# Kernel tuning notes

Hardware: AMD Instinct MI355X
Metric: run time of the kernel (lower is better)

Reference implementation:

```python
import jax, jax.numpy as jnp
import numpy as np

B, D, H, W = 16, 128, 64, 64
K = 512  # num_embeddings


def setup_inputs() -> dict:
    key = jax.random.key(0)
    k1, k2 = jax.random.split(key)
    inputs = jax.random.normal(k1, (B, D, H, W), dtype=jnp.float32)
    embedding_weight = jax.random.normal(k2, (K, D), dtype=jnp.float32)
    return {"inputs": inputs, "embedding_weight": embedding_weight}


def reference(inputs, embedding_weight):
    # NCHW -> NHWC, flatten to [N, D]
    x = jnp.transpose(inputs, (0, 2, 3, 1))  # [B, H, W, D]
    flat = x.reshape(-1, x.shape[-1])        # [N, D]
    dists = (
        jnp.sum(flat ** 2, axis=1, keepdims=True)
        + jnp.sum(embedding_weight ** 2, axis=1)
        - 2.0 * flat @ embedding_weight.T
    )  # [N, K]
    idx = jnp.argmin(dists, axis=1)          # [N]
    # one-hot @ codebook == gather
    quantized = embedding_weight[idx].reshape(x.shape)  # [B, H, W, D]
    # straight-through estimator
    quantized = x + jax.lax.stop_gradient(quantized - x)
    return jnp.transpose(quantized, (0, 3, 1, 2))  # back to NCHW
```

## Files before the change

kernel.cpp:

```cpp
#include <hip/hip_runtime.h>


typedef _Float16 f16;
typedef _Float16 f16x4 __attribute__((ext_vector_type(4)));
typedef _Float16 f16x8 __attribute__((ext_vector_type(8)));
typedef float f32x16 __attribute__((ext_vector_type(16)));

#define ND 128
#define NK 512
#define NHW 4096
#define LO_SCALE 2048.0f
#define LO_INV (1.0f / 2048.0f)

#define WS_EHI 0
#define WS_ELO 131072u
#define WS_ENS 262144u
#define WS_NEED 264192u

__global__ __launch_bounds__(256) void vq_prep_e(const float* __restrict__ e,
                                                 f16* __restrict__ ehi, f16* __restrict__ elo,
                                                 float* __restrict__ ens) {
  const int tid = threadIdx.x;
  const int k0 = (int)blockIdx.x * 16;
  const int r = tid >> 4, dq16 = tid & 15;
  const int k = k0 + r;
  float ssum = 0.0f;
  #pragma unroll
  for (int hh = 0; hh < 2; ++hh) {
    const int dq = dq16 + 16 * hh;
    const float4 v = *(const float4*)(e + (size_t)k * ND + 4 * dq);
    ssum += v.x * v.x + v.y * v.y + v.z * v.z + v.w * v.w;
    float va[4] = {v.x, v.y, v.z, v.w};
    f16x4 hv, lv;
    #pragma unroll
    for (int j = 0; j < 4; ++j) {
      const f16 h = (f16)va[j];
      hv[j] = h;
      lv[j] = (f16)((va[j] - (float)h) * LO_SCALE);
    }
    const int sl = (dq >> 1) ^ (k & 15);
    const size_t off = (size_t)k * ND + sl * 8 + (dq & 1) * 4;
    *(f16x4*)(ehi + off) = hv;
    *(f16x4*)(elo + off) = lv;
  }
  #pragma unroll
  for (int m = 1; m < 16; m <<= 1) ssum += __shfl_xor(ssum, m, 64);
  if (dq16 == 0) ens[k] = 0.5f * ssum;
}

__global__ __launch_bounds__(256) void vq_score(const float* __restrict__ x,
                                                const f16* __restrict__ ehi,
                                                const f16* __restrict__ elo,
                                                const float* __restrict__ ens,
                                                const float* __restrict__ e32,
                                                float* __restrict__ out) {
  __shared__ f16 eh_s[64 * 128];
  __shared__ f16 el_s[64 * 128];
  __shared__ float ens_s[NK];

  const int tid = threadIdx.x;
  const int w = tid >> 6;
  const int lane = tid & 63;
  const int l31 = lane & 31;
  const int half = lane >> 5;
  const int T0 = (int)blockIdx.x * 128;
  const int tok = T0 + w * 32 + l31;
  const int bb = tok >> 12;
  const int hw = tok & 4095;

  #pragma unroll
  for (int p = 0; p < 4; ++p) {
    __builtin_amdgcn_global_load_lds(ehi + p * 2048 + tid * 8, &eh_s[p * 2048 + tid * 8], 16, 0, 0);
    __builtin_amdgcn_global_load_lds(elo + p * 2048 + tid * 8, &el_s[p * 2048 + tid * 8], 16, 0, 0);
  }

  f16x8 Bh[8], Bl[8];
  {
    const float* xb = x + (size_t)bb * ND * NHW + hw;
    #pragma unroll
    for (int ks = 0; ks < 8; ++ks) {
      const int oct = 2 * ks + half;
      #pragma unroll
      for (int j = 0; j < 8; ++j) {
        const float v = xb[(size_t)(oct * 8 + j) * NHW];
        const f16 hv = (f16)v;
        Bh[ks][j] = hv;
        Bl[ks][j] = (f16)((v - (float)hv) * LO_SCALE);
      }
    }
  }
  ens_s[tid] = ens[tid];
  ens_s[tid + 256] = ens[tid + 256];
  __syncthreads();

  float bv = -3.0e38f;
  int bi = 0;
  const int sbase = l31 & 15;

  for (int c = 0; c < 8; ++c) {
    #pragma unroll
    for (int cg = 0; cg < 2; ++cg) {
      const int r = cg * 32 + l31;
      const f16* ah = &eh_s[r * 128];
      const f16* al = &el_s[r * 128];
      f32x16 a1 = {}, a2 = {};
      __builtin_amdgcn_s_setprio(1);
      #pragma unroll
      for (int ks = 0; ks < 8; ++ks) {
        const int sl = ((2 * ks + half) ^ sbase) * 8;
        const f16x8 Ah = *(const f16x8*)(ah + sl);
        const f16x8 Al = *(const f16x8*)(al + sl);
        a2 = __builtin_amdgcn_mfma_f32_32x32x16_f16(Al, Bh[ks], a2, 0, 0, 0);
        a1 = __builtin_amdgcn_mfma_f32_32x32x16_f16(Ah, Bh[ks], a1, 0, 0, 0);
        a2 = __builtin_amdgcn_mfma_f32_32x32x16_f16(Ah, Bl[ks], a2, 0, 0, 0);
      }
      __builtin_amdgcn_s_setprio(0);
      const int kb = c * 64 + cg * 32 + 4 * half;
      const float4 b0 = *(const float4*)&ens_s[kb + 0];
      const float4 b1 = *(const float4*)&ens_s[kb + 8];
      const float4 b2 = *(const float4*)&ens_s[kb + 16];
      const float4 b3 = *(const float4*)&ens_s[kb + 24];
      const float bias[16] = {b0.x, b0.y, b0.z, b0.w, b1.x, b1.y, b1.z, b1.w,
                              b2.x, b2.y, b2.z, b2.w, b3.x, b3.y, b3.z, b3.w};
      #pragma unroll
      for (int rr = 0; rr < 16; ++rr) {
        const float s = a1[rr] + a2[rr] * LO_INV - bias[rr];
        const int code = kb + (rr & 3) + 8 * (rr >> 2);
        if (s > bv) { bv = s; bi = code; }
      }
    }
    __syncthreads();
    if (c < 7) {
      const f16* gh = ehi + (c + 1) * 8192;
      const f16* gl = elo + (c + 1) * 8192;
      #pragma unroll
      for (int p = 0; p < 4; ++p) {
        __builtin_amdgcn_global_load_lds(gh + p * 2048 + tid * 8, &eh_s[p * 2048 + tid * 8], 16, 0, 0);
        __builtin_amdgcn_global_load_lds(gl + p * 2048 + tid * 8, &el_s[p * 2048 + tid * 8], 16, 0, 0);
      }
      __syncthreads();
    }
  }

  {
    const float ov = __shfl_xor(bv, 32, 64);
    const int oi = __shfl_xor(bi, 32, 64);
    if (ov > bv || (ov == bv && oi < bi)) { bv = ov; bi = oi; }
  }

  {
    const float* er = e32 + (size_t)bi * ND + half * 64;
    float* ob = out + (size_t)bb * ND * NHW + (size_t)(half * 64) * NHW + hw;
    #pragma unroll
    for (int j4 = 0; j4 < 16; ++j4) {
      const float4 ev = *(const float4*)(er + j4 * 4);
      ob[(size_t)(j4 * 4 + 0) * NHW] = ev.x;
      ob[(size_t)(j4 * 4 + 1) * NHW] = ev.y;
      ob[(size_t)(j4 * 4 + 2) * NHW] = ev.z;
      ob[(size_t)(j4 * 4 + 3) * NHW] = ev.w;
    }
  }
}

__global__ __launch_bounds__(128) void vq_enorm(const float* __restrict__ e,
                                                float* __restrict__ ensw) {
  const int k = blockIdx.x;
  const int d = threadIdx.x;
  const float v = e[k * ND + d];
  float s = v * v;
  #pragma unroll
  for (int off = 32; off > 0; off >>= 1) s += __shfl_down(s, off, 64);
  __shared__ float tmp[2];
  if ((d & 63) == 0) tmp[d >> 6] = s;
  __syncthreads();
  if (d == 0) ensw[k] = tmp[0] + tmp[1];
}

__global__ __launch_bounds__(256, 2) void vq_main_f32(const float* __restrict__ x,
                                                      const float* __restrict__ e,
                                                      const float* __restrict__ ensw,
                                                      float* __restrict__ out) {
  __shared__ float xs[ND][64];
  __shared__ float esh[ND][64];
  __shared__ float enh[NK];
  __shared__ float red_v[64][17];
  __shared__ int red_i[64][17];
  __shared__ int bidx[64];
  const int tid = threadIdx.x;
  const int b = blockIdx.x >> 6;
  const int hw0 = (blockIdx.x & 63) * 64;
  const float* xb = x + ((size_t)b * ND) * NHW;
  #pragma unroll
  for (int i = 0; i < 8; ++i) {
    const int f = tid + 256 * i;
    const int d = f >> 4, t4 = f & 15;
    const float4 v = *(const float4*)(xb + (size_t)d * NHW + hw0 + 4 * t4);
    *(float4*)&xs[d][4 * t4] = v;
  }
  #pragma unroll
  for (int i = 0; i < 2; ++i) enh[tid + 256 * i] = ensw[tid + 256 * i];
  const int t4 = tid & 15, m = tid >> 4;
  float bvv[4] = {-3.0e38f, -3.0e38f, -3.0e38f, -3.0e38f};
  int bii[4] = {0, 0, 0, 0};
  for (int kc = 0; kc < NK / 64; ++kc) {
    __syncthreads();
    #pragma unroll
    for (int i = 0; i < 8; ++i) {
      const int f = tid + 256 * i;
      const int kk = f & 63, dq = f >> 6;
      const float4 v = *(const float4*)(e + (size_t)(kc * 64 + kk) * ND + 4 * dq);
      esh[4 * dq + 0][kk] = v.x; esh[4 * dq + 1][kk] = v.y;
      esh[4 * dq + 2][kk] = v.z; esh[4 * dq + 3][kk] = v.w;
    }
    __syncthreads();
    float acc[4][4];
    #pragma unroll
    for (int a = 0; a < 4; ++a)
      #pragma unroll
      for (int cc = 0; cc < 4; ++cc) acc[a][cc] = 0.0f;
    #pragma unroll 8
    for (int d = 0; d < ND; ++d) {
      const float4 xv = *(const float4*)&xs[d][4 * t4];
      const float4 ev = *(const float4*)&esh[d][4 * m];
      const float xa[4] = {xv.x, xv.y, xv.z, xv.w};
      const float ea[4] = {ev.x, ev.y, ev.z, ev.w};
      #pragma unroll
      for (int a = 0; a < 4; ++a)
        #pragma unroll
        for (int cc = 0; cc < 4; ++cc) acc[a][cc] = fmaf(xa[a], ea[cc], acc[a][cc]);
    }
    const int kbase = kc * 64 + 4 * m;
    #pragma unroll
    for (int cc = 0; cc < 4; ++cc) {
      const float bias = 0.5f * enh[kbase + cc];
      const int kg = kbase + cc;
      #pragma unroll
      for (int a = 0; a < 4; ++a) {
        const float s = acc[a][cc] - bias;
        if (s > bvv[a] || (s == bvv[a] && kg < bii[a])) { bvv[a] = s; bii[a] = kg; }
      }
    }
  }
  #pragma unroll
  for (int a = 0; a < 4; ++a) { red_v[4 * t4 + a][m] = bvv[a]; red_i[4 * t4 + a][m] = bii[a]; }
  __syncthreads();
  if (tid < 64) {
    float v = red_v[tid][0]; int ix = red_i[tid][0];
    #pragma unroll
    for (int j = 1; j < 16; ++j) {
      const float vj = red_v[tid][j]; const int ij = red_i[tid][j];
      if (vj > v || (vj == v && ij < ix)) { v = vj; ix = ij; }
    }
    bidx[tid] = ix;
  }
  __syncthreads();
  const int t = tid & 63, dgg = tid >> 6;
  const float* er = e + (size_t)bidx[t] * ND;
  float* ob = out + ((size_t)b * ND) * NHW + hw0 + t;
  #pragma unroll
  for (int i = 0; i < 32; ++i) ob[(size_t)(dgg * 32 + i) * NHW] = er[dgg * 32 + i];
}

extern "C" void kernel_launch(void* const* d_in, const int* in_sizes, int n_in,
                              void* d_out, int out_size, void* d_ws, size_t ws_size,
                              hipStream_t stream) {
  const float* x = (const float*)d_in[0];
  const float* e = (const float*)d_in[1];
  float* out = (float*)d_out;
  char* ws = (char*)d_ws;

  if (ws_size >= WS_NEED) {
    f16* ehi = (f16*)(ws + WS_EHI);
    f16* elo = (f16*)(ws + WS_ELO);
    float* ens = (float*)(ws + WS_ENS);
    vq_prep_e<<<32, 256, 0, stream>>>(e, ehi, elo, ens);
    vq_score<<<512, 256, 0, stream>>>(x, ehi, elo, ens, e, out);
  } else {
    float* ensw = (float*)d_ws;
    vq_enorm<<<NK, 128, 0, stream>>>(e, ensw);
    vq_main_f32<<<16 * 64, 256, 0, stream>>>(x, e, ensw, out);
  }
}
```

Measured before the change: 45.45 us.

## Split codebook across two blocks per token tile with atomic argmin merge

The scoring kernel now splits the 512-entry codebook into two halves, so each token tile is handled by two blocks and the grid doubles to 1024 blocks. Each block packs its best score and index into a 64-bit monotone key, and the blocks combine results with atomicMax into a workspace buffer that the prep kernel zeroes. A new scatter kernel reads the winning index and writes the gathered codebook rows to the NCHW output. The aim is more parallelism and occupancy. The cost is that each half recomputes the x fp16 hi/lo split, and the change adds atomics and an extra kernel launch.

```diff
diff --git a/kernel.cpp b/kernel.cpp
--- a/kernel.cpp
+++ b/kernel.cpp
@@ -15,12 +15,23 @@
 #define WS_EHI 0
 #define WS_ELO 131072u
 #define WS_ENS 262144u
-#define WS_NEED 264192u
+#define WS_WIN 264192u
+#define WS_NEED 788480u
+
+__device__ __forceinline__ unsigned mono_key(float v) {
+  const unsigned u = __float_as_uint(v);
+  return (u & 0x80000000u) ? ~u : (u | 0x80000000u);
+}
 
 __global__ __launch_bounds__(256) void vq_prep_e(const float* __restrict__ e,
                                                  f16* __restrict__ ehi, f16* __restrict__ elo,
-                                                 float* __restrict__ ens) {
+                                                 float* __restrict__ ens,
+                                                 unsigned long long* __restrict__ win) {
   const int tid = threadIdx.x;
+  if (blockIdx.x >= 32) {
+    win[((int)blockIdx.x - 32) * 256 + tid] = 0ull;
+    return;
+  }
   const int k0 = (int)blockIdx.x * 16;
   const int r = tid >> 4, dq16 = tid & 15;
   const int k = k0 + r;
@@ -52,26 +63,30 @@
                                                 const f16* __restrict__ ehi,
                                                 const f16* __restrict__ elo,
                                                 const float* __restrict__ ens,
-                                                const float* __restrict__ e32,
-                                                float* __restrict__ out) {
+                                                unsigned long long* __restrict__ win) {
   __shared__ f16 eh_s[64 * 128];
   __shared__ f16 el_s[64 * 128];
-  __shared__ float ens_s[NK];
+  __shared__ float ens_s[256];
+  __shared__ unsigned long long cand[128][5];
 
   const int tid = threadIdx.x;
   const int w = tid >> 6;
   const int lane = tid & 63;
   const int l31 = lane & 31;
   const int half = lane >> 5;
-  const int T0 = (int)blockIdx.x * 128;
+  const int tile = (int)blockIdx.x >> 1;
+  const int bc = (int)blockIdx.x & 1;
+  const int T0 = tile * 128;
   const int tok = T0 + w * 32 + l31;
   const int bb = tok >> 12;
   const int hw = tok & 4095;
+  const f16* eh0 = ehi + (size_t)bc * 4 * 8192;
+  const f16* el0 = elo + (size_t)bc * 4 * 8192;
 
   #pragma unroll
   for (int p = 0; p < 4; ++p) {
-    __builtin_amdgcn_global_load_lds(ehi + p * 2048 + tid * 8, &eh_s[p * 2048 + tid * 8], 16, 0, 0);
-    __builtin_amdgcn_global_load_lds(elo + p * 2048 + tid * 8, &el_s[p * 2048 + tid * 8], 16, 0, 0);
+    __builtin_amdgcn_global_load_lds(eh0 + p * 2048 + tid * 8, &eh_s[p * 2048 + tid * 8], 16, 0, 0);
+    __builtin_amdgcn_global_load_lds(el0 + p * 2048 + tid * 8, &el_s[p * 2048 + tid * 8], 16, 0, 0);
   }
 
   f16x8 Bh[8], Bl[8];
@@ -89,15 +104,14 @@
       }
     }
   }
-  ens_s[tid] = ens[tid];
-  ens_s[tid + 256] = ens[tid + 256];
+  ens_s[tid] = ens[bc * 256 + tid];
   __syncthreads();
 
   float bv = -3.0e38f;
   int bi = 0;
   const int sbase = l31 & 15;
 
-  for (int c = 0; c < 8; ++c) {
+  for (int c = 0; c < 4; ++c) {
     #pragma unroll
     for (int cg = 0; cg < 2; ++cg) {
       const int r = cg * 32 + l31;
@@ -130,9 +144,9 @@
       }
     }
     __syncthreads();
-    if (c < 7) {
-      const f16* gh = ehi + (c + 1) * 8192;
-      const f16* gl = elo + (c + 1) * 8192;
+    if (c < 3) {
+      const f16* gh = eh0 + (c + 1) * 8192;
+      const f16* gl = el0 + (c + 1) * 8192;
       #pragma unroll
       for (int p = 0; p < 4; ++p) {
         __builtin_amdgcn_global_load_lds(gh + p * 2048 + tid * 8, &eh_s[p * 2048 + tid * 8], 16, 0, 0);
@@ -147,18 +161,38 @@
     const int oi = __shfl_xor(bi, 32, 64);
     if (ov > bv || (ov == bv && oi < bi)) { bv = ov; bi = oi; }
   }
-
-  {
-    const float* er = e32 + (size_t)bi * ND + half * 64;
-    float* ob = out + (size_t)bb * ND * NHW + (size_t)(half * 64) * NHW + hw;
-    #pragma unroll
-    for (int j4 = 0; j4 < 16; ++j4) {
-      const float4 ev = *(const float4*)(er + j4 * 4);
-      ob[(size_t)(j4 * 4 + 0) * NHW] = ev.x;
-      ob[(size_t)(j4 * 4 + 1) * NHW] = ev.y;
-      ob[(size_t)(j4 * 4 + 2) * NHW] = ev.z;
-      ob[(size_t)(j4 * 4 + 3) * NHW] = ev.w;
-    }
+  const int gcode = bc * 256 + bi;
+  const unsigned long long key =
+      ((unsigned long long)mono_key(bv) << 32) | (unsigned)(511 - gcode);
+
+  if (half == 0) cand[w * 32 + l31][w] = key;
+  __syncthreads();
+  if (tid < 128) {
+    atomicMax(win + T0 + tid, cand[tid][tid >> 5]);
+  }
+}
+
+__global__ __launch_bounds__(256) void vq_scatter(const unsigned long long* __restrict__ win,
+                                                  const float* __restrict__ e32,
+                                                  float* __restrict__ out) {
+  __shared__ int bidx_s[64];
+  const int tid = threadIdx.x;
+  const int T0 = (int)blockIdx.x * 64;
+  if (tid < 64) bidx_s[tid] = 511 - (int)(win[T0 + tid] & 0x1FFull);
+  __syncthreads();
+  const int tloc = tid & 63, dg = tid >> 6;
+  const int Tg = T0 + tloc;
+  const int bb = Tg >> 12;
+  const int hw = Tg & 4095;
+  const float* er = e32 + (size_t)bidx_s[tloc] * ND + dg * 32;
+  float* ob = out + (size_t)bb * ND * NHW + (size_t)(dg * 32) * NHW + hw;
+  #pragma unroll
+  for (int j4 = 0; j4 < 8; ++j4) {
+    const float4 ev = *(const float4*)(er + j4 * 4);
+    ob[(size_t)(j4 * 4 + 0) * NHW] = ev.x;
+    ob[(size_t)(j4 * 4 + 1) * NHW] = ev.y;
+    ob[(size_t)(j4 * 4 + 2) * NHW] = ev.z;
+    ob[(size_t)(j4 * 4 + 3) * NHW] = ev.w;
   }
 }
 
@@ -273,8 +307,10 @@
     f16* ehi = (f16*)(ws + WS_EHI);
     f16* elo = (f16*)(ws + WS_ELO);
     float* ens = (float*)(ws + WS_ENS);
-    vq_prep_e<<<32, 256, 0, stream>>>(e, ehi, elo, ens);
-    vq_score<<<512, 256, 0, stream>>>(x, ehi, elo, ens, e, out);
+    unsigned long long* win = (unsigned long long*)(ws + WS_WIN);
+    vq_prep_e<<<288, 256, 0, stream>>>(e, ehi, elo, ens, win);
+    vq_score<<<1024, 256, 0, stream>>>(x, ehi, elo, ens, win);
+    vq_scatter<<<1024, 256, 0, stream>>>(win, e, out);
   } else {
     float* ensw = (float*)d_ws;
     vq_enorm<<<NK, 128, 0, stream>>>(e, ensw);
```

Result: slower. 50.76 us (+11.7%).

## Double-buffer codebook chunks and split codebook halves across wave pairs

Applied to the files above, without the earlier changes.

The score kernel moves to 512 threads. Each pair of waves covers the same 32 tokens, with one wave scanning codebook chunks 0-3 and the other chunks 4-7. Codebook tiles are now double-buffered in LDS, so the next chunk's global-to-LDS load is issued before the current chunk is scored, removing one barrier per chunk. The per-half argmins are merged through shared memory using monotone packed keys that keep the lowest index on ties, and the output gather-write is spread over all 512 threads. The cost is twice the LDS per block (lower occupancy), duplicated x loads per wave pair, and waves that sit idle during the chunks they do not own.

```diff
diff --git a/kernel.cpp b/kernel.cpp
--- a/kernel.cpp
+++ b/kernel.cpp
@@ -16,6 +16,11 @@
 #define WS_ELO 131072u
 #define WS_ENS 262144u
 #define WS_NEED 264192u
+
+__device__ __forceinline__ unsigned mono_key(float v) {
+  const unsigned u = __float_as_uint(v);
+  return (u & 0x80000000u) ? ~u : (u | 0x80000000u);
+}
 
 __global__ __launch_bounds__(256) void vq_prep_e(const float* __restrict__ e,
                                                  f16* __restrict__ ehi, f16* __restrict__ elo,
@@ -48,30 +53,34 @@
   if (dq16 == 0) ens[k] = 0.5f * ssum;
 }
 
-__global__ __launch_bounds__(256) void vq_score(const float* __restrict__ x,
+__global__ __launch_bounds__(512) void vq_score(const float* __restrict__ x,
                                                 const f16* __restrict__ ehi,
                                                 const f16* __restrict__ elo,
                                                 const float* __restrict__ ens,
                                                 const float* __restrict__ e32,
                                                 float* __restrict__ out) {
-  __shared__ f16 eh_s[64 * 128];
-  __shared__ f16 el_s[64 * 128];
+  __shared__ f16 eh_s[2][64 * 128];
+  __shared__ f16 el_s[2][64 * 128];
   __shared__ float ens_s[NK];
+  __shared__ unsigned long long cand[128][2];
+  __shared__ int bidx_s[128];
 
   const int tid = threadIdx.x;
   const int w = tid >> 6;
   const int lane = tid & 63;
   const int l31 = lane & 31;
   const int half = lane >> 5;
+  const int tpair = w >> 1;
+  const int myhalf = w & 1;
   const int T0 = (int)blockIdx.x * 128;
-  const int tok = T0 + w * 32 + l31;
+  const int tok = T0 + tpair * 32 + l31;
   const int bb = tok >> 12;
   const int hw = tok & 4095;
 
   #pragma unroll
-  for (int p = 0; p < 4; ++p) {
-    __builtin_amdgcn_global_load_lds(ehi + p * 2048 + tid * 8, &eh_s[p * 2048 + tid * 8], 16, 0, 0);
-    __builtin_amdgcn_global_load_lds(elo + p * 2048 + tid * 8, &el_s[p * 2048 + tid * 8], 16, 0, 0);
+  for (int p = 0; p < 2; ++p) {
+    __builtin_amdgcn_global_load_lds(ehi + p * 4096 + tid * 8, &eh_s[0][p * 4096 + tid * 8], 16, 0, 0);
+    __builtin_amdgcn_global_load_lds(elo + p * 4096 + tid * 8, &el_s[0][p * 4096 + tid * 8], 16, 0, 0);
   }
 
   f16x8 Bh[8], Bl[8];
@@ -90,56 +99,60 @@
     }
   }
   ens_s[tid] = ens[tid];
-  ens_s[tid + 256] = ens[tid + 256];
   __syncthreads();
 
   float bv = -3.0e38f;
   int bi = 0;
+  int cur = 0;
   const int sbase = l31 & 15;
 
   for (int c = 0; c < 8; ++c) {
-    #pragma unroll
-    for (int cg = 0; cg < 2; ++cg) {
-      const int r = cg * 32 + l31;
-      const f16* ah = &eh_s[r * 128];
-      const f16* al = &el_s[r * 128];
-      f32x16 a1 = {}, a2 = {};
-      __builtin_amdgcn_s_setprio(1);
-      #pragma unroll
-      for (int ks = 0; ks < 8; ++ks) {
-        const int sl = ((2 * ks + half) ^ sbase) * 8;
-        const f16x8 Ah = *(const f16x8*)(ah + sl);
-        const f16x8 Al = *(const f16x8*)(al + sl);
-        a2 = __builtin_amdgcn_mfma_f32_32x32x16_f16(Al, Bh[ks], a2, 0, 0, 0);
-        a1 = __builtin_amdgcn_mfma_f32_32x32x16_f16(Ah, Bh[ks], a1, 0, 0, 0);
-        a2 = __builtin_amdgcn_mfma_f32_32x32x16_f16(Ah, Bl[ks], a2, 0, 0, 0);
-      }
-      __builtin_amdgcn_s_setprio(0);
-      const int kb = c * 64 + cg * 32 + 4 * half;
-      const float4 b0 = *(const float4*)&ens_s[kb + 0];
-      const float4 b1 = *(const float4*)&ens_s[kb + 8];
-      const float4 b2 = *(const float4*)&ens_s[kb + 16];
-      const float4 b3 = *(const float4*)&ens_s[kb + 24];
-      const float bias[16] = {b0.x, b0.y, b0.z, b0.w, b1.x, b1.y, b1.z, b1.w,
-                              b2.x, b2.y, b2.z, b2.w, b3.x, b3.y, b3.z, b3.w};
-      #pragma unroll
-      for (int rr = 0; rr < 16; ++rr) {
-        const float s = a1[rr] + a2[rr] * LO_INV - bias[rr];
-        const int code = kb + (rr & 3) + 8 * (rr >> 2);
-        if (s > bv) { bv = s; bi = code; }
-      }
-    }
-    __syncthreads();
     if (c < 7) {
       const f16* gh = ehi + (c + 1) * 8192;
       const f16* gl = elo + (c + 1) * 8192;
-      #pragma unroll
-      for (int p = 0; p < 4; ++p) {
-        __builtin_amdgcn_global_load_lds(gh + p * 2048 + tid * 8, &eh_s[p * 2048 + tid * 8], 16, 0, 0);
-        __builtin_amdgcn_global_load_lds(gl + p * 2048 + tid * 8, &el_s[p * 2048 + tid * 8], 16, 0, 0);
+      f16* dh = &eh_s[cur ^ 1][0];
+      f16* dl = &el_s[cur ^ 1][0];
+      #pragma unroll
+      for (int p = 0; p < 2; ++p) {
+        __builtin_amdgcn_global_load_lds(gh + p * 4096 + tid * 8, dh + p * 4096 + tid * 8, 16, 0, 0);
+        __builtin_amdgcn_global_load_lds(gl + p * 4096 + tid * 8, dl + p * 4096 + tid * 8, 16, 0, 0);
       }
-      __syncthreads();
-    }
+    }
+    if ((c >> 2) == myhalf) {
+      #pragma unroll
+      for (int cg = 0; cg < 2; ++cg) {
+        const int r = cg * 32 + l31;
+        const f16* ah = &eh_s[cur][r * 128];
+        const f16* al = &el_s[cur][r * 128];
+        f32x16 a1 = {}, a2 = {};
+        __builtin_amdgcn_s_setprio(1);
+        #pragma unroll
+        for (int ks = 0; ks < 8; ++ks) {
+          const int sl = ((2 * ks + half) ^ sbase) * 8;
+          const f16x8 Ah = *(const f16x8*)(ah + sl);
+          const f16x8 Al = *(const f16x8*)(al + sl);
+          a2 = __builtin_amdgcn_mfma_f32_32x32x16_f16(Al, Bh[ks], a2, 0, 0, 0);
+          a1 = __builtin_amdgcn_mfma_f32_32x32x16_f16(Ah, Bh[ks], a1, 0, 0, 0);
+          a2 = __builtin_amdgcn_mfma_f32_32x32x16_f16(Ah, Bl[ks], a2, 0, 0, 0);
+        }
+        __builtin_amdgcn_s_setprio(0);
+        const int kb = c * 64 + cg * 32 + 4 * half;
+        const float4 b0 = *(const float4*)&ens_s[kb + 0];
+        const float4 b1 = *(const float4*)&ens_s[kb + 8];
+        const float4 b2 = *(const float4*)&ens_s[kb + 16];
+        const float4 b3 = *(const float4*)&ens_s[kb + 24];
+        const float bias[16] = {b0.x, b0.y, b0.z, b0.w, b1.x, b1.y, b1.z, b1.w,
+                                b2.x, b2.y, b2.z, b2.w, b3.x, b3.y, b3.z, b3.w};
+        #pragma unroll
+        for (int rr = 0; rr < 16; ++rr) {
+          const float s = a1[rr] + a2[rr] * LO_INV - bias[rr];
+          const int code = kb + (rr & 3) + 8 * (rr >> 2);
+          if (s > bv) { bv = s; bi = code; }
+        }
+      }
+    }
+    __syncthreads();
+    cur ^= 1;
   }
 
   {
@@ -147,12 +160,26 @@
     const int oi = __shfl_xor(bi, 32, 64);
     if (ov > bv || (ov == bv && oi < bi)) { bv = ov; bi = oi; }
   }
+  const unsigned long long key =
+      ((unsigned long long)mono_key(bv) << 32) | (unsigned)(511 - bi);
+  if (half == 0) cand[tpair * 32 + l31][myhalf] = key;
+  __syncthreads();
+  if (tid < 128) {
+    const unsigned long long k0 = cand[tid][0];
+    const unsigned long long k1 = cand[tid][1];
+    bidx_s[tid] = 511 - (int)(((k1 > k0) ? k1 : k0) & 0x1FFull);
+  }
+  __syncthreads();
 
   {
-    const float* er = e32 + (size_t)bi * ND + half * 64;
-    float* ob = out + (size_t)bb * ND * NHW + (size_t)(half * 64) * NHW + hw;
-    #pragma unroll
-    for (int j4 = 0; j4 < 16; ++j4) {
+    const int tl = tid & 127, dg = tid >> 7;
+    const int Tg = T0 + tl;
+    const int obb = Tg >> 12;
+    const int ohw = Tg & 4095;
+    const float* er = e32 + (size_t)bidx_s[tl] * ND + dg * 32;
+    float* ob = out + (size_t)obb * ND * NHW + (size_t)(dg * 32) * NHW + ohw;
+    #pragma unroll
+    for (int j4 = 0; j4 < 8; ++j4) {
       const float4 ev = *(const float4*)(er + j4 * 4);
       ob[(size_t)(j4 * 4 + 0) * NHW] = ev.x;
       ob[(size_t)(j4 * 4 + 1) * NHW] = ev.y;
@@ -274,7 +301,7 @@
     f16* elo = (f16*)(ws + WS_ELO);
     float* ens = (float*)(ws + WS_ENS);
     vq_prep_e<<<32, 256, 0, stream>>>(e, ehi, elo, ens);
-    vq_score<<<512, 256, 0, stream>>>(x, ehi, elo, ens, e, out);
+    vq_score<<<512, 512, 0, stream>>>(x, ehi, elo, ens, e, out);
   } else {
     float* ensw = (float*)d_ws;
     vq_enorm<<<NK, 128, 0, stream>>>(e, ensw);
```

Result: slower. 64.30 us (+41.5%).
